# Performance work log

Measured on AMD Instinct MI355X. Metric: run time of the kernel, lower is better.

The kernel has to match this reference:

```python
import jax, jax.numpy as jnp
import numpy as np

NUM_HEADS = 16


def setup_inputs() -> dict:
    key = jax.random.key(0)
    ks = jax.random.split(key, 5)
    B, S, D = 2, 2048, 1024
    scale = 0.02
    return {
        "x": jax.random.normal(ks[0], (B, S, D), dtype=jnp.float32),
        "Wq": jax.random.normal(ks[1], (D, D), dtype=jnp.float32) * scale,
        "Wk": jax.random.normal(ks[2], (D, D), dtype=jnp.float32) * scale,
        "Wv": jax.random.normal(ks[3], (D, D), dtype=jnp.float32) * scale,
        "Wo": jax.random.normal(ks[4], (D, D), dtype=jnp.float32) * scale,
        "bo": jnp.zeros((D,), dtype=jnp.float32),
    }


def reference(x, Wq, Wk, Wv, Wo, bo):
    B, S, D = x.shape
    H = NUM_HEADS
    Dh = D // H
    # project and split heads -> [B, H, S, Dh]
    q = (x @ Wq).reshape(B, S, H, Dh).transpose(0, 2, 1, 3)
    k = (x @ Wk).reshape(B, S, H, Dh).transpose(0, 2, 1, 3)
    v = (x @ Wv).reshape(B, S, H, Dh).transpose(0, 2, 1, 3)
    # full causal attention scores [B, H, S, S]
    scores = jnp.einsum("bhqd,bhkd->bhqk", q, k)
    causal_mask = jnp.triu(jnp.ones((S, S), dtype=bool), k=1)
    scores = jnp.where(causal_mask, -jnp.inf, scores)
    attn = jax.nn.softmax(scores / jnp.sqrt(jnp.float32(Dh)), axis=-1)
    ctx = jnp.einsum("bhqk,bhkd->bhqd", attn, v)
    ctx = ctx.transpose(0, 2, 1, 3).reshape(B, S, D)
    return ctx @ Wo + bo
```

## Files before the change

### kernel.cpp

```cpp
#include <hip/hip_runtime.h>
#include <hip/hip_bf16.h>
#include <math.h>

typedef __bf16 bf16_t;
typedef bf16_t bf16x4 __attribute__((ext_vector_type(4)));
typedef bf16_t bf16x8 __attribute__((ext_vector_type(8)));
typedef float f32x4 __attribute__((ext_vector_type(4)));

#define MFMA16(a, b, c) __builtin_amdgcn_mfma_f32_16x16x32_bf16(a, b, c, 0, 0, 0)
#define NEG_BIG (-1e30f)

#define GLL16(gp, lp)                                                          \
    __builtin_amdgcn_global_load_lds(                                          \
        (const __attribute__((address_space(1))) unsigned int*)(gp),           \
        (__attribute__((address_space(3))) unsigned int*)(lp), 16, 0, 0)


__global__ __launch_bounds__(256) void cvt_bf16(const float* __restrict__ in,
                                                bf16_t* __restrict__ out, int n) {
    int i = (blockIdx.x * 256 + threadIdx.x) * 4;
    if (i < n) {
        float4 v = *(const float4*)(in + i);
        out[i + 0] = (bf16_t)v.x;
        out[i + 1] = (bf16_t)v.y;
        out[i + 2] = (bf16_t)v.z;
        out[i + 3] = (bf16_t)v.w;
    }
}

__global__ __launch_bounds__(256) void transpose_w(const float* __restrict__ W,
                                                   bf16_t* __restrict__ WT) {
    __shared__ float tile[32][33];
    int bx = blockIdx.x * 32, by = blockIdx.y * 32;
    int tx = threadIdx.x, ty = threadIdx.y;
    for (int i = 0; i < 32; i += 8)
        tile[ty + i][tx] = W[(size_t)(by + ty + i) * 1024 + bx + tx];
    __syncthreads();
    for (int i = 0; i < 32; i += 8)
        WT[(size_t)(bx + ty + i) * 1024 + by + tx] = (bf16_t)tile[tx][ty + i];
}

__global__ __launch_bounds__(256) void gemm_qkv(const bf16_t* __restrict__ X,
                                                const bf16_t* __restrict__ WT,
                                                bf16_t* __restrict__ Qd,
                                                bf16_t* __restrict__ Kd,
                                                bf16_t* __restrict__ Vd) {
    __shared__ bf16_t AsmF[128 * 64];
    __shared__ bf16_t BsmF[128 * 64];
    const int which = blockIdx.z;
    const bf16_t* Wt = WT + (size_t)which * 1024 * 1024;
    const int bm = blockIdx.y * 128;
    const int bn = blockIdx.x * 128;
    const int tid = threadIdx.x;
    const int wave = tid >> 6, lane = tid & 63;
    const int wm = (wave >> 1) * 64, wn = (wave & 1) * 64;
    const int col = lane & 15, quad = lane >> 4;
    const int cswz = col & 7;
    const int lr8 = lane >> 3;
    const int jg = (lane & 7) ^ lr8;

    const int srow = wave * 32 + lr8;
    const bf16_t* gA = X  + (size_t)(bm + srow) * 1024 + jg * 8;
    const bf16_t* gB = Wt + (size_t)(bn + srow) * 1024 + jg * 8;
    bf16_t* lA = AsmF + wave * 2048;
    bf16_t* lB = BsmF + wave * 2048;

    f32x4 acc[4][4] = {};

    for (int k0 = 0; k0 < 1024; k0 += 64) {
        for (int j = 0; j < 4; j++) {
            GLL16(gA + (size_t)j * 8192 + k0, lA + j * 512);
            GLL16(gB + (size_t)j * 8192 + k0, lB + j * 512);
        }
        __syncthreads();
        for (int ks = 0; ks < 2; ks++) {
            bf16x8 af[4], bfr[4];
            for (int mi = 0; mi < 4; mi++)
                af[mi] = *(const bf16x8*)&AsmF[(wm + mi * 16 + col) * 64 +
                                               (((ks << 2) + quad) ^ cswz) * 8];
            for (int ni = 0; ni < 4; ni++)
                bfr[ni] = *(const bf16x8*)&BsmF[(wn + ni * 16 + col) * 64 +
                                                (((ks << 2) + quad) ^ cswz) * 8];
            if (which != 2) {
                for (int mi = 0; mi < 4; mi++)
                    for (int ni = 0; ni < 4; ni++)
                        acc[mi][ni] = MFMA16(af[mi], bfr[ni], acc[mi][ni]);
            } else {
                for (int mi = 0; mi < 4; mi++)
                    for (int ni = 0; ni < 4; ni++)
                        acc[mi][ni] = MFMA16(bfr[ni], af[mi], acc[mi][ni]);
            }
        }
        __syncthreads();
    }

    if (which != 2) {
        for (int mi = 0; mi < 4; mi++) {
            for (int ni = 0; ni < 4; ni++) {
                int mbase = bm + wm + mi * 16 + quad * 4;
                int n = bn + wn + ni * 16 + col;
                int h = n >> 6, dh = n & 63;
                for (int r = 0; r < 4; r++) {
                    int m = mbase + r;
                    int b = m >> 11, s = m & 2047;
                    size_t bh = (size_t)b * 16 + h;
                    bf16_t val = (bf16_t)acc[mi][ni][r];
                    if (which == 0) Qd[(bh * 2048 + s) * 64 + dh] = val;
                    else            Kd[(bh * 2048 + s) * 64 + dh] = val;
                }
            }
        }
    } else {
        for (int mi = 0; mi < 4; mi++) {
            for (int ni = 0; ni < 4; ni++) {
                int nbase = bn + wn + ni * 16 + quad * 4;
                int m = bm + wm + mi * 16 + col;
                int b = m >> 11, s = m & 2047;
                for (int r = 0; r < 4; r++) {
                    int n = nbase + r;
                    int h = n >> 6, dh = n & 63;
                    size_t bh = (size_t)b * 16 + h;
                    Vd[(bh * 64 + dh) * 2048 + s] = (bf16_t)acc[mi][ni][r];
                }
            }
        }
    }
}

#define PSD 72
__global__ __launch_bounds__(256) void attn(const bf16_t* __restrict__ Q,
                                            const bf16_t* __restrict__ K,
                                            const bf16_t* __restrict__ VT,
                                            bf16_t* __restrict__ CTX) {
    __shared__ bf16_t KsF[2 * 64 * 64];
    __shared__ bf16_t VsF[2 * 64 * 64];
    __shared__ bf16_t Ps[4][16][PSD];

    const int bh = blockIdx.y;
    const int pr = blockIdx.x;
    const int tid = threadIdx.x;
    const int wave = tid >> 6, lane = tid & 63;
    const int col = lane & 15, quad = lane >> 4;
    const int cswz = col & 7;
    const int lr8 = lane >> 3;
    const int jg = (lane & 7) ^ lr8;

    const bf16_t* Qb = Q + (size_t)bh * 2048 * 64;
    const bf16_t* Kb = K + (size_t)bh * 2048 * 64;
    const bf16_t* Vb = VT + (size_t)bh * 64 * 2048;

    const int strow = wave * 16 + lr8;
    const bf16_t* gK = Kb + (size_t)strow * 64 + jg * 8;
    const bf16_t* gV = Vb + (size_t)strow * 2048 + jg * 8;

    const int b_ = bh >> 4, h_ = bh & 15;

    int g = 0;
    for (int ph = 0; ph < 2; ph++) {
        const int qt = ph ? (31 - pr) : pr;
        const int q0 = qt * 64;

        const int qrow = q0 + wave * 16 + col;
        const bf16x8 qf0 = *(const bf16x8*)&Qb[(size_t)qrow * 64 + quad * 8];
        const bf16x8 qf1 = *(const bf16x8*)&Qb[(size_t)qrow * 64 + 32 + quad * 8];

        f32x4 o[4] = {};
        float lsum = 0.f;

        const int nt = qt + 1;
        for (int t = 0; t < nt; t++, g++) {
            const int bsel = g & 1;
            const int k0 = t * 64;
            bf16_t* lK = KsF + bsel * 4096 + wave * 1024;
            bf16_t* lV = VsF + bsel * 4096 + wave * 1024;
            for (int j = 0; j < 2; j++) {
                GLL16(gK + (size_t)(k0 + j * 8) * 64, lK + j * 512);
                GLL16(gV + (size_t)(k0 + j * 8 * 2048), lV + j * 512);
            }
            __syncthreads();

            const bool diag = (t == qt);
            const bf16_t* Kbuf = KsF + bsel * 4096;
            const bf16_t* Vbuf = VsF + bsel * 4096;
            for (int ksub = 0; ksub < 4; ksub++) {
                bf16x8 a0 = *(const bf16x8*)&Kbuf[(ksub * 16 + col) * 64 +
                                                  (quad ^ cswz) * 8];
                bf16x8 a1 = *(const bf16x8*)&Kbuf[(ksub * 16 + col) * 64 +
                                                  ((4 + quad) ^ cswz) * 8];
                f32x4 z = {};
                z = MFMA16(a0, qf0, z);
                z = MFMA16(a1, qf1, z);
                if (diag) {
                    for (int r = 0; r < 4; r++) {
                        int lk = ksub * 16 + quad * 4 + r;
                        if (lk > wave * 16 + col) z[r] = NEG_BIG;
                    }
                }
                bf16x4 pw;
                for (int r = 0; r < 4; r++) {
                    float p = __expf(z[r] * 0.125f);
                    lsum += p;
                    pw[r] = (bf16_t)p;
                }
                *(bf16x4*)&Ps[wave][col][ksub * 16 + quad * 4] = pw;
            }

            for (int ck = 0; ck < 2; ck++) {
                bf16x8 pf = *(const bf16x8*)&Ps[wave][col][ck * 32 + quad * 8];
                for (int d = 0; d < 4; d++) {
                    bf16x8 vf = *(const bf16x8*)&Vbuf[(d * 16 + col) * 64 +
                                                      (((ck << 2) + quad) ^ cswz) * 8];
                    o[d] = MFMA16(pf, vf, o[d]);
                }
            }
        }

        float lt = lsum + __shfl_xor(lsum, 16, 64);
        lt += __shfl_xor(lt, 32, 64);
        float lq[4];
        for (int r = 0; r < 4; r++)
            lq[r] = __shfl(lt, quad * 4 + r, 64);

        for (int d = 0; d < 4; d++) {
            for (int r = 0; r < 4; r++) {
                int s = q0 + wave * 16 + quad * 4 + r;
                int dh = d * 16 + col;
                CTX[((size_t)(b_ * 2048 + s)) * 1024 + h_ * 64 + dh] =
                    (bf16_t)(o[d][r] / fmaxf(lq[r], 1e-20f));
            }
        }
        __syncthreads();
    }
}

__global__ __launch_bounds__(256) void gemm_out(const bf16_t* __restrict__ X,
                                                const bf16_t* __restrict__ WT,
                                                const float* __restrict__ BO,
                                                float* __restrict__ OUT) {
    __shared__ bf16_t AsmF[64 * 64];
    __shared__ bf16_t BsmF[128 * 64];
    const int bm = blockIdx.y * 64;
    const int bn = blockIdx.x * 128;
    const int tid = threadIdx.x;
    const int wave = tid >> 6, lane = tid & 63;
    const int wm = (wave >> 1) * 32, wn = (wave & 1) * 64;
    const int col = lane & 15, quad = lane >> 4;
    const int cswz = col & 7;
    const int lr8 = lane >> 3;
    const int jg = (lane & 7) ^ lr8;

    const int arow = wave * 16 + lr8;
    const int brow = wave * 32 + lr8;
    const bf16_t* gA = X  + (size_t)(bm + arow) * 1024 + jg * 8;
    const bf16_t* gB = WT + (size_t)(bn + brow) * 1024 + jg * 8;
    bf16_t* lA = AsmF + wave * 1024;
    bf16_t* lB = BsmF + wave * 2048;

    f32x4 acc[2][4] = {};

    for (int k0 = 0; k0 < 1024; k0 += 64) {
        for (int j = 0; j < 2; j++)
            GLL16(gA + (size_t)j * 8192 + k0, lA + j * 512);
        for (int j = 0; j < 4; j++)
            GLL16(gB + (size_t)j * 8192 + k0, lB + j * 512);
        __syncthreads();
        for (int ks = 0; ks < 2; ks++) {
            bf16x8 af[2], bfr[4];
            for (int mi = 0; mi < 2; mi++)
                af[mi] = *(const bf16x8*)&AsmF[(wm + mi * 16 + col) * 64 +
                                               (((ks << 2) + quad) ^ cswz) * 8];
            for (int ni = 0; ni < 4; ni++)
                bfr[ni] = *(const bf16x8*)&BsmF[(wn + ni * 16 + col) * 64 +
                                                (((ks << 2) + quad) ^ cswz) * 8];
            for (int mi = 0; mi < 2; mi++)
                for (int ni = 0; ni < 4; ni++)
                    acc[mi][ni] = MFMA16(af[mi], bfr[ni], acc[mi][ni]);
        }
        __syncthreads();
    }

    for (int mi = 0; mi < 2; mi++) {
        for (int ni = 0; ni < 4; ni++) {
            int mbase = bm + wm + mi * 16 + quad * 4;
            int n = bn + wn + ni * 16 + col;
            float bov = BO[n];
            for (int r = 0; r < 4; r++) {
                int m = mbase + r;
                OUT[(size_t)m * 1024 + n] = acc[mi][ni][r] + bov;
            }
        }
    }
}

extern "C" void kernel_launch(void* const* d_in, const int* in_sizes, int n_in,
                              void* d_out, int out_size, void* d_ws, size_t ws_size,
                              hipStream_t stream) {
    const float* x  = (const float*)d_in[0];
    const float* Wq = (const float*)d_in[1];
    const float* Wk = (const float*)d_in[2];
    const float* Wv = (const float*)d_in[3];
    const float* Wo = (const float*)d_in[4];
    const float* bo = (const float*)d_in[5];
    float* out = (float*)d_out;

    const size_t MEG = 1048576;
    bf16_t* base  = (bf16_t*)d_ws;
    bf16_t* Xb    = base;
    bf16_t* WTqkv = base + 4 * MEG;
    bf16_t* WoT   = base + 7 * MEG;
    bf16_t* Qb    = base + 8 * MEG;
    bf16_t* Kb    = base + 12 * MEG;
    bf16_t* Vb    = base + 16 * MEG;
    bf16_t* Cb    = base + 20 * MEG;

    cvt_bf16<<<4096, 256, 0, stream>>>(x, Xb, 4 * MEG);

    dim3 tb(32, 8);
    transpose_w<<<dim3(32, 32), tb, 0, stream>>>(Wq, WTqkv);
    transpose_w<<<dim3(32, 32), tb, 0, stream>>>(Wk, WTqkv + 1 * MEG);
    transpose_w<<<dim3(32, 32), tb, 0, stream>>>(Wv, WTqkv + 2 * MEG);
    transpose_w<<<dim3(32, 32), tb, 0, stream>>>(Wo, WoT);

    gemm_qkv<<<dim3(8, 32, 3), 256, 0, stream>>>(Xb, WTqkv, Qb, Kb, Vb);
    attn<<<dim3(16, 32), 256, 0, stream>>>(Qb, Kb, Vb, Cb);
    gemm_out<<<dim3(8, 64), 256, 0, stream>>>(Cb, WoT, bo, out);
}
```

Before: 192.5 us.

## Fuse prep kernels and software-pipeline attention K/V loads across both query tiles

The five conversion and transpose launches become a single prep kernel that picks its job from blockIdx.z, which removes launch overhead. The attention kernel now runs its two causal query tiles as one 33-step loop. The next K/V tile is issued through global_load_lds before the current tile's compute, so loads overlap with MFMA work instead of stalling at the barrier. It also switches __expf to exp2f with a folded log2e scale and flattens the grid so consecutive blocks take different heads. The risk is that the single sync per step must still correctly protect the double buffer.

```diff
diff --git a/kernel.cpp b/kernel.cpp
--- a/kernel.cpp
+++ b/kernel.cpp
@@ -16,28 +16,37 @@
         (__attribute__((address_space(3))) unsigned int*)(lp), 16, 0, 0)
 
 
-__global__ __launch_bounds__(256) void cvt_bf16(const float* __restrict__ in,
-                                                bf16_t* __restrict__ out, int n) {
-    int i = (blockIdx.x * 256 + threadIdx.x) * 4;
-    if (i < n) {
-        float4 v = *(const float4*)(in + i);
-        out[i + 0] = (bf16_t)v.x;
-        out[i + 1] = (bf16_t)v.y;
-        out[i + 2] = (bf16_t)v.z;
-        out[i + 3] = (bf16_t)v.w;
-    }
-}
-
-__global__ __launch_bounds__(256) void transpose_w(const float* __restrict__ W,
-                                                   bf16_t* __restrict__ WT) {
+__global__ __launch_bounds__(256) void prep(const float* __restrict__ x,
+                                            const float* __restrict__ Wq,
+                                            const float* __restrict__ Wk,
+                                            const float* __restrict__ Wv,
+                                            const float* __restrict__ Wo,
+                                            bf16_t* __restrict__ Xb,
+                                            bf16_t* __restrict__ WTqkv,
+                                            bf16_t* __restrict__ WoT) {
     __shared__ float tile[32][33];
-    int bx = blockIdx.x * 32, by = blockIdx.y * 32;
-    int tx = threadIdx.x, ty = threadIdx.y;
-    for (int i = 0; i < 32; i += 8)
-        tile[ty + i][tx] = W[(size_t)(by + ty + i) * 1024 + bx + tx];
-    __syncthreads();
-    for (int i = 0; i < 32; i += 8)
-        WT[(size_t)(bx + ty + i) * 1024 + by + tx] = (bf16_t)tile[tx][ty + i];
+    const int z = blockIdx.z;
+    const int tx = threadIdx.x, ty = threadIdx.y;
+    if (z == 4) {
+        int i0 = (((blockIdx.y * 32 + blockIdx.x) * 256) + ty * 32 + tx) * 4;
+        for (int j = 0; j < 4; j++) {
+            int i = i0 + j * 1048576;
+            float4 v = *(const float4*)(x + i);
+            Xb[i + 0] = (bf16_t)v.x;
+            Xb[i + 1] = (bf16_t)v.y;
+            Xb[i + 2] = (bf16_t)v.z;
+            Xb[i + 3] = (bf16_t)v.w;
+        }
+    } else {
+        const float* W = (z == 0) ? Wq : (z == 1) ? Wk : (z == 2) ? Wv : Wo;
+        bf16_t* WT = (z < 3) ? (WTqkv + (size_t)z * 1048576) : WoT;
+        int bx = blockIdx.x * 32, by = blockIdx.y * 32;
+        for (int i = 0; i < 32; i += 8)
+            tile[ty + i][tx] = W[(size_t)(by + ty + i) * 1024 + bx + tx];
+        __syncthreads();
+        for (int i = 0; i < 32; i += 8)
+            WT[(size_t)(bx + ty + i) * 1024 + by + tx] = (bf16_t)tile[tx][ty + i];
+    }
 }
 
 __global__ __launch_bounds__(256) void gemm_qkv(const bf16_t* __restrict__ X,
@@ -136,8 +145,10 @@
     __shared__ bf16_t VsF[2 * 64 * 64];
     __shared__ bf16_t Ps[4][16][PSD];
 
-    const int bh = blockIdx.y;
-    const int pr = blockIdx.x;
+    const int bidx = blockIdx.x;
+    const int bh = bidx & 31;
+    const int pr = bidx >> 5;
+    const int qt0 = pr, qt1 = 31 - pr;
     const int tid = threadIdx.x;
     const int wave = tid >> 6, lane = tid & 63;
     const int col = lane & 15, quad = lane >> 4;
@@ -155,81 +166,99 @@
 
     const int b_ = bh >> 4, h_ = bh & 15;
 
-    int g = 0;
-    for (int ph = 0; ph < 2; ph++) {
-        const int qt = ph ? (31 - pr) : pr;
-        const int q0 = qt * 64;
-
-        const int qrow = q0 + wave * 16 + col;
-        const bf16x8 qf0 = *(const bf16x8*)&Qb[(size_t)qrow * 64 + quad * 8];
-        const bf16x8 qf1 = *(const bf16x8*)&Qb[(size_t)qrow * 64 + 32 + quad * 8];
-
-        f32x4 o[4] = {};
-        float lsum = 0.f;
-
-        const int nt = qt + 1;
-        for (int t = 0; t < nt; t++, g++) {
-            const int bsel = g & 1;
-            const int k0 = t * 64;
-            bf16_t* lK = KsF + bsel * 4096 + wave * 1024;
-            bf16_t* lV = VsF + bsel * 4096 + wave * 1024;
-            for (int j = 0; j < 2; j++) {
-                GLL16(gK + (size_t)(k0 + j * 8) * 64, lK + j * 512);
-                GLL16(gV + (size_t)(k0 + j * 8 * 2048), lV + j * 512);
-            }
-            __syncthreads();
-
-            const bool diag = (t == qt);
-            const bf16_t* Kbuf = KsF + bsel * 4096;
-            const bf16_t* Vbuf = VsF + bsel * 4096;
-            for (int ksub = 0; ksub < 4; ksub++) {
-                bf16x8 a0 = *(const bf16x8*)&Kbuf[(ksub * 16 + col) * 64 +
-                                                  (quad ^ cswz) * 8];
-                bf16x8 a1 = *(const bf16x8*)&Kbuf[(ksub * 16 + col) * 64 +
-                                                  ((4 + quad) ^ cswz) * 8];
-                f32x4 z = {};
-                z = MFMA16(a0, qf0, z);
-                z = MFMA16(a1, qf1, z);
-                if (diag) {
-                    for (int r = 0; r < 4; r++) {
-                        int lk = ksub * 16 + quad * 4 + r;
-                        if (lk > wave * 16 + col) z[r] = NEG_BIG;
-                    }
+    auto stage = [&](int k0, int bsel) {
+        bf16_t* lK = KsF + bsel * 4096 + wave * 1024;
+        bf16_t* lV = VsF + bsel * 4096 + wave * 1024;
+        for (int j = 0; j < 2; j++) {
+            GLL16(gK + (size_t)(k0 + j * 8) * 64, lK + j * 512);
+            GLL16(gV + (size_t)(k0 + j * 8 * 2048), lV + j * 512);
+        }
+    };
+
+    stage(0, 0);
+
+    int q0 = qt0 * 64;
+    int qrow = q0 + wave * 16 + col;
+    bf16x8 qf0 = *(const bf16x8*)&Qb[(size_t)qrow * 64 + quad * 8];
+    bf16x8 qf1 = *(const bf16x8*)&Qb[(size_t)qrow * 64 + 32 + quad * 8];
+
+    f32x4 o[4] = {};
+    float lsum = 0.f;
+
+    for (int g = 0; g < 33; g++) {
+        __syncthreads();
+        if (g < 32) {
+            int gn = g + 1;
+            int k0n = (gn <= qt0 ? gn : gn - qt0 - 1) * 64;
+            stage(k0n, gn & 1);
+        }
+
+        const int bsel = g & 1;
+        const bf16_t* Kbuf = KsF + bsel * 4096;
+        const bf16_t* Vbuf = VsF + bsel * 4096;
+        const bool diag = (g == qt0) || (g == 32);
+
+        for (int ksub = 0; ksub < 4; ksub++) {
+            bf16x8 a0 = *(const bf16x8*)&Kbuf[(ksub * 16 + col) * 64 +
+                                              (quad ^ cswz) * 8];
+            bf16x8 a1 = *(const bf16x8*)&Kbuf[(ksub * 16 + col) * 64 +
+                                              ((4 + quad) ^ cswz) * 8];
+            f32x4 z = {};
+            z = MFMA16(a0, qf0, z);
+            z = MFMA16(a1, qf1, z);
+            if (diag) {
+                for (int r = 0; r < 4; r++) {
+                    int lk = ksub * 16 + quad * 4 + r;
+                    if (lk > wave * 16 + col) z[r] = NEG_BIG;
                 }
-                bf16x4 pw;
+            }
+            bf16x4 pw;
+            for (int r = 0; r < 4; r++) {
+                float p = exp2f(z[r] * 0.18033688f);
+                lsum += p;
+                pw[r] = (bf16_t)p;
+            }
+            *(bf16x4*)&Ps[wave][col][ksub * 16 + quad * 4] = pw;
+        }
+
+        for (int ck = 0; ck < 2; ck++) {
+            bf16x8 pf = *(const bf16x8*)&Ps[wave][col][ck * 32 + quad * 8];
+            for (int d = 0; d < 4; d++) {
+                bf16x8 vf = *(const bf16x8*)&Vbuf[(d * 16 + col) * 64 +
+                                                  (((ck << 2) + quad) ^ cswz) * 8];
+                o[d] = MFMA16(pf, vf, o[d]);
+            }
+        }
+
+        if (g == qt0) {
+            float lt = lsum + __shfl_xor(lsum, 16, 64);
+            lt += __shfl_xor(lt, 32, 64);
+            for (int d = 0; d < 4; d++) {
                 for (int r = 0; r < 4; r++) {
-                    float p = __expf(z[r] * 0.125f);
-                    lsum += p;
-                    pw[r] = (bf16_t)p;
+                    float lq = __shfl(lt, quad * 4 + r, 64);
+                    int s = q0 + wave * 16 + quad * 4 + r;
+                    CTX[((size_t)(b_ * 2048 + s)) * 1024 + h_ * 64 + d * 16 + col] =
+                        (bf16_t)(o[d][r] / fmaxf(lq, 1e-20f));
                 }
-                *(bf16x4*)&Ps[wave][col][ksub * 16 + quad * 4] = pw;
-            }
-
-            for (int ck = 0; ck < 2; ck++) {
-                bf16x8 pf = *(const bf16x8*)&Ps[wave][col][ck * 32 + quad * 8];
-                for (int d = 0; d < 4; d++) {
-                    bf16x8 vf = *(const bf16x8*)&Vbuf[(d * 16 + col) * 64 +
-                                                      (((ck << 2) + quad) ^ cswz) * 8];
-                    o[d] = MFMA16(pf, vf, o[d]);
-                }
-            }
-        }
-
-        float lt = lsum + __shfl_xor(lsum, 16, 64);
-        lt += __shfl_xor(lt, 32, 64);
-        float lq[4];
-        for (int r = 0; r < 4; r++)
-            lq[r] = __shfl(lt, quad * 4 + r, 64);
-
-        for (int d = 0; d < 4; d++) {
-            for (int r = 0; r < 4; r++) {
-                int s = q0 + wave * 16 + quad * 4 + r;
-                int dh = d * 16 + col;
-                CTX[((size_t)(b_ * 2048 + s)) * 1024 + h_ * 64 + dh] =
-                    (bf16_t)(o[d][r] / fmaxf(lq[r], 1e-20f));
-            }
-        }
-        __syncthreads();
+                o[d] = f32x4{};
+            }
+            lsum = 0.f;
+            q0 = qt1 * 64;
+            qrow = q0 + wave * 16 + col;
+            qf0 = *(const bf16x8*)&Qb[(size_t)qrow * 64 + quad * 8];
+            qf1 = *(const bf16x8*)&Qb[(size_t)qrow * 64 + 32 + quad * 8];
+        }
+    }
+
+    float lt = lsum + __shfl_xor(lsum, 16, 64);
+    lt += __shfl_xor(lt, 32, 64);
+    for (int d = 0; d < 4; d++) {
+        for (int r = 0; r < 4; r++) {
+            float lq = __shfl(lt, quad * 4 + r, 64);
+            int s = q0 + wave * 16 + quad * 4 + r;
+            CTX[((size_t)(b_ * 2048 + s)) * 1024 + h_ * 64 + d * 16 + col] =
+                (bf16_t)(o[d][r] / fmaxf(lq, 1e-20f));
+        }
     }
 }
 
@@ -313,15 +342,9 @@
     bf16_t* Vb    = base + 16 * MEG;
     bf16_t* Cb    = base + 20 * MEG;
 
-    cvt_bf16<<<4096, 256, 0, stream>>>(x, Xb, 4 * MEG);
-
-    dim3 tb(32, 8);
-    transpose_w<<<dim3(32, 32), tb, 0, stream>>>(Wq, WTqkv);
-    transpose_w<<<dim3(32, 32), tb, 0, stream>>>(Wk, WTqkv + 1 * MEG);
-    transpose_w<<<dim3(32, 32), tb, 0, stream>>>(Wv, WTqkv + 2 * MEG);
-    transpose_w<<<dim3(32, 32), tb, 0, stream>>>(Wo, WoT);
-
+    prep<<<dim3(32, 32, 5), dim3(32, 8), 0, stream>>>(x, Wq, Wk, Wv, Wo,
+                                                      Xb, WTqkv, WoT);
     gemm_qkv<<<dim3(8, 32, 3), 256, 0, stream>>>(Xb, WTqkv, Qb, Kb, Vb);
-    attn<<<dim3(16, 32), 256, 0, stream>>>(Qb, Kb, Vb, Cb);
+    attn<<<512, 256, 0, stream>>>(Qb, Kb, Vb, Cb);
     gemm_out<<<dim3(8, 64), 256, 0, stream>>>(Cb, WoT, bo, out);
 }
```

Result: no change. 192.6 us (+0.0%).
